# Optimization experiments

Measured on AMD Instinct MI355X. Metric: run time of the kernel, lower is better.

The kernel has to match this reference:

```python
import jax, jax.numpy as jnp
import numpy as np

B, N, IN_DIM, HID, K = 8, 4096, 10, 64, 8
NORM = np.array([1.0/2950.0, 1.0/2950.0, 1.0/2950.0, 1.0/5.265625, 1.0/143.875,
                 1.0/589.0, 1.0/1.2050781, 1.0/211.0, 1.0, 1.0/7.0], dtype=np.float32)


def _lin(key, fan_in, fan_out):
    k1, k2 = jax.random.split(key)
    s = 1.0 / np.sqrt(fan_in)
    w = jax.random.uniform(k1, (fan_in, fan_out), jnp.float32, -s, s)
    b = jax.random.uniform(k2, (fan_out,), jnp.float32, -s, s)
    return w, b


def setup_inputs() -> dict:
    key = jax.random.key(0)
    ks = jax.random.split(key, 10)
    x = jax.random.normal(ks[0], (B, N, IN_DIM), jnp.float32)
    w_in1, b_in1 = _lin(ks[1], IN_DIM, HID // 2)
    w_in2, b_in2 = _lin(ks[2], HID // 2, HID)
    w_c1a, b_c1a = _lin(ks[3], 2 * HID, 3 * HID // 2)
    w_c1b, b_c1b = _lin(ks[4], 3 * HID // 2, HID)
    w_c2a, b_c2a = _lin(ks[5], 2 * HID, 3 * HID // 2)
    w_c2b, b_c2b = _lin(ks[6], 3 * HID // 2, HID)
    w_o1, b_o1 = _lin(ks[7], HID, HID)
    w_o2, b_o2 = _lin(ks[8], HID, HID // 2)
    w_o3, b_o3 = _lin(ks[9], HID // 2, 2)
    return dict(x=x, datanorm=jnp.asarray(NORM),
                w_in1=w_in1, b_in1=b_in1, w_in2=w_in2, b_in2=b_in2,
                w_c1a=w_c1a, b_c1a=b_c1a, w_c1b=w_c1b, b_c1b=b_c1b,
                w_c2a=w_c2a, b_c2a=b_c2a, w_c2b=w_c2b, b_c2b=b_c2b,
                w_o1=w_o1, b_o1=b_o1, w_o2=w_o2, b_o2=b_o2, w_o3=w_o3, b_o3=b_o3)


def _knn(x, k):
    # x: [B, n, H] -> [B, n, k] indices of k nearest neighbors (self excluded)
    x2 = jnp.sum(x * x, -1)
    d = x2[:, :, None] + x2[:, None, :] - 2.0 * jnp.einsum('bnh,bmh->bnm', x, x)
    n = x.shape[1]
    d = d + jnp.eye(n, dtype=x.dtype) * 1e9
    return jax.lax.top_k(-d, k)[1]


def _edge_conv(x, nbr, w1, b1, w2, b2):
    # EdgeConv with max aggregation over undirected kNN edges.
    # message(i <- j) = MLP([x_i, x_j - x_i]); edges symmetrized (j->i and i->j).
    b, n, k = nbr.shape
    dst0 = jnp.broadcast_to(jnp.arange(n)[None, :, None], (b, n, k)).reshape(b, n * k)
    src0 = nbr.reshape(b, n * k)
    src = jnp.concatenate([src0, dst0], 1)  # [b, 2nk]
    dst = jnp.concatenate([dst0, src0], 1)
    xd = jnp.take_along_axis(x, dst[..., None], 1)
    xs = jnp.take_along_axis(x, src[..., None], 1)
    m = jnp.concatenate([xd, xs - xd], -1)           # [b, 2nk, 2H]
    m = jax.nn.elu(m @ w1 + b1)
    m = jax.nn.elu(m @ w2 + b2)
    seg = lambda mm, dd: jax.ops.segment_max(mm, dd, num_segments=n)
    return jax.vmap(seg)(m, dst)                     # [b, n, H]


def reference(x, datanorm, w_in1, b_in1, w_in2, b_in2,
              w_c1a, b_c1a, w_c1b, b_c1b, w_c2a, b_c2a, w_c2b, b_c2b,
              w_o1, b_o1, w_o2, b_o2, w_o3, b_o3):
    h = x * datanorm
    h = jax.nn.elu(h @ w_in1 + b_in1)
    h = jax.nn.elu(h @ w_in2 + b_in2)
    nbr = _knn(jax.lax.stop_gradient(h), K)          # knn_graph is non-differentiable
    h = _edge_conv(h, nbr, w_c1a, b_c1a, w_c1b, b_c1b)
    # deterministic pairwise max-pool (stand-in for graclus+max_pool, halves node count)
    h = h.reshape(B, N // 2, 2, HID).max(2)
    nbr = _knn(jax.lax.stop_gradient(h), K)
    h = _edge_conv(h, nbr, w_c2a, b_c2a, w_c2b, b_c2b)
    # second graclus max_pool_x followed by global_max_pool == global max pool
    g = h.max(1)                                     # [B, HID]
    o = jax.nn.elu(g @ w_o1 + b_o1)
    o = jax.nn.elu(o @ w_o2 + b_o2)
    o = o @ w_o3 + b_o3                              # [B, 2]
    met = jax.nn.softplus(o[:, :1])
    metphi = jnp.pi * (2.0 * jax.nn.sigmoid(o[:, 1:2]) - 1.0)
    return jnp.concatenate([met, metphi], 1)
```

## Files before the change

kernel.cpp:

```cpp
#include <hip/hip_runtime.h>
#include <hip/hip_bf16.h>

#define BATCH 8
#define N1 4096
#define N2 2048
#define HID 64
#define KNN 8
#define INDIM 10

using u64 = unsigned long long;
using bf16 = __hip_bfloat16;
typedef __attribute__((ext_vector_type(8))) short short8;
typedef __attribute__((ext_vector_type(4))) float f32x4;

__device__ __align__(256) float    g_h1[BATCH * N1 * HID];
__device__ __align__(256) float    g_h2[BATCH * N2 * HID];
__device__ __align__(256) float    g_x2n[BATCH * N1];
__device__ __align__(256) float    g_x2n2[BATCH * N2];
__device__ __align__(256) int      g_nbr[BATCH * N1 * KNN];
__device__ __align__(256) float    g_uu[BATCH * N1 * 96];
__device__ __align__(256) float    g_vv[BATCH * N1 * 96];
__device__ __align__(256) unsigned g_ek1[BATCH * N1 * HID];
__device__ __align__(256) unsigned g_ek2[BATCH * N2 * HID];
__device__ __align__(256) short    g_f1[BATCH * N1 * HID];
__device__ __align__(256) short    g_f2[BATCH * N1 * HID];
__device__ __align__(256) short    g_f3[BATCH * N1 * HID];
__device__ __align__(256) float    g_uf[BATCH * N1 * 96];
__device__ __align__(256) float    g_vf[BATCH * N1 * 96];
__device__ __align__(256) short    g_wf1[2 * 4 * 3 * 64 * 8];
__device__ __align__(256) short    g_wf2[2 * 4 * 3 * 64 * 8];

__device__ __forceinline__ float eluf(float x) { return x > 0.f ? x : __expf(x) - 1.f; }
__device__ __forceinline__ unsigned encf(float f) {
  unsigned u = __float_as_uint(f);
  return u ^ ((unsigned)((int)u >> 31) | 0x80000000u);
}
__device__ __forceinline__ float decf(unsigned k) {
  unsigned u = (k & 0x80000000u) ? (k & 0x7FFFFFFFu) : ~k;
  return __uint_as_float(u);
}
#define ENC_NEG1 0x407FFFFFu
__device__ __forceinline__ unsigned enc_safe(float v) {
  if (!(v == v)) return ENC_NEG1;
  return encf(v);
}
__device__ __forceinline__ float dec_safe(unsigned k) {
  float v = decf(k);
  if (!(v == v)) return -1.0f;
  return fminf(fmaxf(v, -3.0e38f), 3.0e38f);
}
__device__ __forceinline__ unsigned umed3(unsigned a, unsigned b, unsigned c) {
  unsigned d;
  asm("v_med3_u32 %0, %1, %2, %3" : "=v"(d) : "v"(a), "v"(b), "v"(c));
  return d;
}
__device__ __forceinline__ void split3(float v, short& b1, short& b2, short& b3) {
  bf16 x1 = __float2bfloat16(v);
  float r1 = v - __bfloat162float(x1);
  bf16 x2 = __float2bfloat16(r1);
  float r2 = r1 - __bfloat162float(x2);
  bf16 x3 = __float2bfloat16(r2);
  b1 = *(short*)&x1; b2 = *(short*)&x2; b3 = *(short*)&x3;
}
__device__ __forceinline__ void split2(float v, short& b1, short& b2) {
  bf16 x1 = __float2bfloat16(v);
  float r1 = v - __bfloat162float(x1);
  bf16 x2 = __float2bfloat16(r1);
  b1 = *(short*)&x1; b2 = *(short*)&x2;
}
__device__ __forceinline__ void store_frags(int node, const short* s1,
                                            const short* s2, const short* s3) {
  size_t tb = ((size_t)(node >> 4)) * 1024 + (node & 15) * 8;
#pragma unroll
  for (int chunk = 0; chunk < 2; ++chunk) {
#pragma unroll
    for (int q = 0; q < 4; ++q) {
      size_t a = tb + chunk * 512 + q * 128;
      int k = chunk * 32 + q * 8;
      *(short8*)(g_f1 + a) = *(const short8*)(s1 + k);
      *(short8*)(g_f2 + a) = *(const short8*)(s2 + k);
      *(short8*)(g_f3 + a) = *(const short8*)(s3 + k);
    }
  }
}
__device__ __forceinline__ void tv_frag(float4 a0, float4 a1, float4 b0,
                                        float4 b1, short8& s1, short8& s2) {
  float v[8] = {a0.x + b0.x, a0.y + b0.y, a0.z + b0.z, a0.w + b0.w,
                a1.x + b1.x, a1.y + b1.y, a1.z + b1.z, a1.w + b1.w};
#pragma unroll
  for (int e = 0; e < 8; ++e) {
    float t = eluf(v[e]);
    short p1, p2;
    split2(t, p1, p2);
    s1[e] = p1; s2[e] = p2;
  }
}

__global__ __launch_bounds__(256) void init_kernel() {
  int t = blockIdx.x * 256 + threadIdx.x;
  uint4 z = make_uint4(ENC_NEG1, ENC_NEG1, ENC_NEG1, ENC_NEG1);
  const int n1 = BATCH * N1 * HID / 4;
  if (t < n1) ((uint4*)g_ek1)[t] = z;
  else ((uint4*)g_ek2)[t - n1] = z;
}

__global__ __launch_bounds__(256) void wfrag_kernel(const float* __restrict__ w1,
                                                    const float* __restrict__ w2) {
  int level = blockIdx.x;
  const float* w = level ? w2 : w1;
  for (int idx = threadIdx.x; idx < 6144; idx += 256) {
    int no = idx / 1536;
    int rem = idx - no * 1536;
    int kc = rem / 512;
    int rem2 = rem - kc * 512;
    int lane = rem2 >> 3;
    int j = rem2 & 7;
    int k = kc * 32 + (lane >> 4) * 8 + j;
    int o = no * 16 + (lane & 15);
    short b1, b2;
    split2(w[k * 64 + o], b1, b2);
    g_wf1[level * 6144 + idx] = b1;
    g_wf2[level * 6144 + idx] = b2;
  }
}

__global__ __launch_bounds__(256) void input_mlp(
    const float* __restrict__ x, const float* __restrict__ norm,
    const float* __restrict__ w1g, const float* __restrict__ b1g,
    const float* __restrict__ w2g, const float* __restrict__ b2g) {
  __shared__ float sw1[320], sb1[32], sw2[2048], sb2[64], snorm[INDIM];
  int t = threadIdx.x;
  for (int q = t; q < 320; q += 256) sw1[q] = w1g[q];
  for (int q = t; q < 2048; q += 256) sw2[q] = w2g[q];
  if (t < 32) sb1[t] = b1g[t];
  if (t < 64) sb2[t] = b2g[t];
  if (t < INDIM) snorm[t] = norm[t];
  __syncthreads();
  int node = blockIdx.x * 256 + t;
  float xv[INDIM];
#pragma unroll
  for (int d = 0; d < INDIM; ++d)
    xv[d] = x[(size_t)node * INDIM + d] * snorm[d];
  float t1[32];
#pragma unroll
  for (int c = 0; c < 32; ++c) {
    float acc = sb1[c];
#pragma unroll
    for (int d = 0; d < INDIM; ++d) acc += xv[d] * sw1[d * 32 + c];
    t1[c] = eluf(acc);
  }
  float* hr = g_h1 + (size_t)node * HID;
  float sq = 0.f;
  short s1l[HID], s2l[HID], s3l[HID];
#pragma unroll
  for (int c = 0; c < HID; ++c) {
    float acc = sb2[c];
#pragma unroll
    for (int d = 0; d < 32; ++d) acc += t1[d] * sw2[d * HID + c];
    float v = eluf(acc);
    hr[c] = v;
    sq += v * v;
    split3(v, s1l[c], s2l[c], s3l[c]);
  }
  store_frags(node, s1l, s2l, s3l);
  g_x2n[node] = sq;
}

template <int LEVEL>
__global__ __launch_bounds__(256, 2) void knn_kernel() {
  constexpr int n = LEVEL ? N2 : N1;
  constexpr int NT = n / 16;
  constexpr int HT = NT / 2;
  constexpr int NSET = LEVEL ? 1 : 2;
  constexpr int SS = NSET * 16;
  __shared__ unsigned lm[32 * 289];

  int b = blockIdx.x & 7;
  int rb = (blockIdx.x >> 3) * (2 * SS);
  int t = threadIdx.x;
  int wv = t >> 6, lane = t & 63;
  int s = wv >> 1, hf = wv & 1;
  int q = lane >> 4, c = lane & 15;
  const float* __restrict__ x2b = (LEVEL ? g_x2n2 : g_x2n) + (size_t)b * n;
  size_t abase = ((size_t)((b * n + rb + s * SS) >> 4)) * 1024 + lane * 8;
  short8 A1a[NSET], A1b[NSET], A2a[NSET], A2b[NSET], A3a[NSET], A3b[NSET];
#pragma unroll
  for (int e = 0; e < NSET; ++e) {
    size_t ab = abase + (size_t)e * 1024;
    A1a[e] = *(const short8*)(g_f1 + ab);
    A1b[e] = *(const short8*)(g_f1 + ab + 512);
    A2a[e] = *(const short8*)(g_f2 + ab);
    A2b[e] = *(const short8*)(g_f2 + ab + 512);
    A3a[e] = *(const short8*)(g_f3 + ab);
    A3b[e] = *(const short8*)(g_f3 + ab + 512);
  }
  unsigned best[NSET][4][KNN];
#pragma unroll
  for (int e = 0; e < NSET; ++e)
#pragma unroll
    for (int r = 0; r < 4; ++r)
#pragma unroll
      for (int p = 0; p < KNN; ++p) best[e][r][p] = 0xFFFFFFFFu;
  const int ct0 = hf * HT;
  const int selftile = (rb + s * SS) >> 4;
  const f32x4 zero = {0.f, 0.f, 0.f, 0.f};
  size_t bb = ((size_t)(b * n) >> 4) * 1024 + (size_t)ct0 * 1024 + lane * 8;

  short8 Pa[6], Pb[6];
  float xa, xb;
  auto LOADB = [&](short8* P, size_t addr) {
    P[0] = *(const short8*)(g_f1 + addr);
    P[1] = *(const short8*)(g_f1 + addr + 512);
    P[2] = *(const short8*)(g_f2 + addr);
    P[3] = *(const short8*)(g_f2 + addr + 512);
    P[4] = *(const short8*)(g_f3 + addr);
    P[5] = *(const short8*)(g_f3 + addr + 512);
  };
  auto COMPUTE = [&](const short8* P, float x2c, int ct) {
#pragma unroll
    for (int e = 0; e < NSET; ++e) {
      f32x4 acc0 = __builtin_amdgcn_mfma_f32_16x16x32_bf16(A1a[e], P[0], zero, 0, 0, 0);
      f32x4 acc1 = __builtin_amdgcn_mfma_f32_16x16x32_bf16(A1b[e], P[1], zero, 0, 0, 0);
      acc0 = __builtin_amdgcn_mfma_f32_16x16x32_bf16(A1a[e], P[2], acc0, 0, 0, 0);
      acc1 = __builtin_amdgcn_mfma_f32_16x16x32_bf16(A1b[e], P[3], acc1, 0, 0, 0);
      acc0 = __builtin_amdgcn_mfma_f32_16x16x32_bf16(A2a[e], P[0], acc0, 0, 0, 0);
      acc1 = __builtin_amdgcn_mfma_f32_16x16x32_bf16(A2b[e], P[1], acc1, 0, 0, 0);
      acc0 = __builtin_amdgcn_mfma_f32_16x16x32_bf16(A1a[e], P[4], acc0, 0, 0, 0);
      acc1 = __builtin_amdgcn_mfma_f32_16x16x32_bf16(A1b[e], P[5], acc1, 0, 0, 0);
      acc0 = __builtin_amdgcn_mfma_f32_16x16x32_bf16(A2a[e], P[2], acc0, 0, 0, 0);
      acc1 = __builtin_amdgcn_mfma_f32_16x16x32_bf16(A2b[e], P[3], acc1, 0, 0, 0);
      acc0 = __builtin_amdgcn_mfma_f32_16x16x32_bf16(A3a[e], P[0], acc0, 0, 0, 0);
      acc1 = __builtin_amdgcn_mfma_f32_16x16x32_bf16(A3b[e], P[1], acc1, 0, 0, 0);
      unsigned ck[4];
#pragma unroll
      for (int r = 0; r < 4; ++r) {
        float sm2 = acc0[r] + acc1[r];
        float dd = __builtin_fmaf(-2.f, sm2, x2c);
        ck[r] = (encf(dd) & 0xFFFFFF00u) | (unsigned)ct;
      }
      if (ct == selftile + e) {
#pragma unroll
        for (int r = 0; r < 4; ++r)
          if (c == q * 4 + r) ck[r] = 0xFFFFFFFFu;
      }
#pragma unroll
      for (int r = 0; r < 4; ++r) {
        unsigned x = ck[r];
#pragma unroll
        for (int p = KNN - 1; p >= 1; --p)
          best[e][r][p] = umed3(best[e][r][p - 1], best[e][r][p], x);
        best[e][r][0] = min(best[e][r][0], x);
      }
    }
  };

  LOADB(Pa, bb);
  xa = x2b[ct0 * 16 + c];
  for (int tt = 0; tt < HT; tt += 2) {
    int ct = ct0 + tt;
    LOADB(Pb, bb + 1024);
    xb = x2b[(ct + 1) * 16 + c];
    COMPUTE(Pa, xa, ct);
    size_t nb2 = (tt + 2 < HT) ? bb + 2048 : bb;
    int ctn2 = (tt + 2 < HT) ? ct + 2 : ct;
    LOADB(Pa, nb2);
    xa = x2b[ctn2 * 16 + c];
    COMPUTE(Pb, xb, ct + 1);
    bb += 2048;
  }
#pragma unroll
  for (int pass = 0; pass < NSET; ++pass) {
#pragma unroll
    for (int r = 0; r < 4; ++r) {
      int lrow = s * 16 + q * 4 + r;
      unsigned* dst = lm + lrow * 289 + (hf * 16 + c) * 9;
#pragma unroll
      for (int p = 0; p < KNN; ++p) dst[p] = best[pass][r][p];
    }
    __syncthreads();
    {
      int arow = t >> 3, am = t & 7;
      unsigned* base = lm + arow * 289;
      const unsigned* l0 = base + (am * 4) * 9;
      u64 fin[KNN];
#pragma unroll
      for (int p = 0; p < KNN; ++p)
        fin[p] = (((u64)l0[p]) << 4) | (unsigned)((am * 4) & 15);
      for (int d = 1; d < 4; ++d) {
        const unsigned* ld = base + (am * 4 + d) * 9;
        unsigned cb = (unsigned)((am * 4 + d) & 15);
        for (int p = 0; p < KNN; ++p) {
          u64 ckk = (((u64)ld[p]) << 4) | cb;
          if (ckk >= fin[KNN - 1]) break;
#pragma unroll
          for (int p2 = 0; p2 < KNN; ++p2) {
            u64 ob = fin[p2];
            bool ex = ob < ckk;
            fin[p2] = ex ? ob : ckk;
            ckk = ex ? ckk : ob;
          }
        }
      }
      unsigned* dst = base + (am * 4) * 9;
#pragma unroll
      for (int p = 0; p < KNN; ++p) {
        dst[2 * p] = (unsigned)fin[p];
        dst[2 * p + 1] = (unsigned)(fin[p] >> 32);
      }
    }
    __syncthreads();
    if (t < 64) {
      int brow = t >> 1, bm = t & 1;
      unsigned* base = lm + brow * 289;
      u64 fin[KNN];
      {
        const unsigned* s0 = base + (bm * 4) * 36;
#pragma unroll
        for (int p = 0; p < KNN; ++p)
          fin[p] = (((u64)s0[2 * p + 1]) << 32) | s0[2 * p];
      }
      for (int d = 1; d < 4; ++d) {
        const unsigned* sd = base + (bm * 4 + d) * 36;
        for (int p = 0; p < KNN; ++p) {
          u64 ckk = (((u64)sd[2 * p + 1]) << 32) | sd[2 * p];
          if (ckk >= fin[KNN - 1]) break;
#pragma unroll
          for (int p2 = 0; p2 < KNN; ++p2) {
            u64 ob = fin[p2];
            bool ex = ob < ckk;
            fin[p2] = ex ? ob : ckk;
            ckk = ex ? ckk : ob;
          }
        }
      }
      unsigned* dst = base + (bm * 4) * 36;
#pragma unroll
      for (int p = 0; p < KNN; ++p) {
        dst[2 * p] = (unsigned)fin[p];
        dst[2 * p + 1] = (unsigned)(fin[p] >> 32);
      }
    }
    __syncthreads();
    if (t < 32) {
      unsigned* base = lm + t * 289;
      u64 fin[KNN];
#pragma unroll
      for (int p = 0; p < KNN; ++p)
        fin[p] = (((u64)base[2 * p + 1]) << 32) | base[2 * p];
      const unsigned* s1 = base + 144;
      for (int p = 0; p < KNN; ++p) {
        u64 ckk = (((u64)s1[2 * p + 1]) << 32) | s1[2 * p];
        if (ckk >= fin[KNN - 1]) break;
#pragma unroll
        for (int p2 = 0; p2 < KNN; ++p2) {
          u64 ob = fin[p2];
          bool ex = ob < ckk;
          fin[p2] = ex ? ob : ckk;
          ckk = ex ? ckk : ob;
        }
      }
      int row = rb + (t >> 4) * SS + pass * 16 + (t & 15);
      int* ob = g_nbr + ((size_t)b * n + row) * KNN;
#pragma unroll
      for (int p = 0; p < KNN; ++p) {
        int j = (int)((fin[p] >> 4) & 255u) * 16 + (int)(fin[p] & 15u);
        ob[p] = j & (n - 1);
      }
    }
    if (pass + 1 < NSET) __syncthreads();
  }
}

__global__ __launch_bounds__(256) void uv_kernel(int level,
                                                 const float* __restrict__ w1g,
                                                 const float* __restrict__ b1g) {
  __shared__ float sw1[128 * 96];
  __shared__ float sb1[96];
  int t = threadIdx.x;
  for (int q = t; q < 128 * 96; q += 256) sw1[q] = w1g[q];
  if (t < 96) sb1[t] = b1g[t];
  __syncthreads();
  const int n = level ? N2 : N1;
  const float* h = level ? g_h2 : g_h1;
  int b = blockIdx.x & 7;
  int nl = (blockIdx.x >> 3) * 64 + (t & 63);
  int c0 = (t >> 6) * 24;
  size_t node = (size_t)b * n + nl;
  const float4* h4 = (const float4*)(h + node * HID);
  float hv[HID];
#pragma unroll
  for (int q = 0; q < 16; ++q) {
    float4 vv = h4[q];
    hv[4 * q] = vv.x; hv[4 * q + 1] = vv.y; hv[4 * q + 2] = vv.z; hv[4 * q + 3] = vv.w;
  }
  float ua[24], va[24];
#pragma unroll
  for (int c = 0; c < 24; ++c) { ua[c] = 0.f; va[c] = 0.f; }
  for (int d = 0; d < HID; ++d) {
    float hd = hv[d];
    const float* wt = sw1 + d * 96 + c0;
    const float* wb = sw1 + (HID + d) * 96 + c0;
#pragma unroll
    for (int c = 0; c < 24; ++c) {
      ua[c] += hd * wt[c];
      va[c] += hd * wb[c];
    }
  }
  float* ur = g_uu + node * 96 + c0;
  float* vr = g_vv + node * 96 + c0;
#pragma unroll
  for (int c = 0; c < 24; ++c) {
    float uval = ua[c] - va[c] + sb1[c0 + c];
    float vval = va[c];
    ur[c] = uval;
    vr[c] = vval;
    int kk = c0 + c;
    size_t fa = (node >> 4) * 1536 + (size_t)((kk >> 5) * 512 +
                ((kk >> 3) & 3) * 128 + (nl & 15) * 8 + (kk & 7));
    g_uf[fa] = uval;
    g_vf[fa] = vval;
  }
}

template <int LEVEL>
__global__ __launch_bounds__(256, 1) void edge_kernel(
    const float* __restrict__ b2g) {
  constexpr int n = LEVEL ? N2 : N1;
  unsigned* ekey = LEVEL ? g_ek2 : g_ek1;
  int b = blockIdx.x & 7;
  int t = threadIdx.x;
  int wv = t >> 6, lane = t & 63;
  int q = lane >> 4, c = lane & 15;
  int base16 = (blockIdx.x >> 3) * 64 + wv * 16;
  int node_c = base16 + c;
  const int* nbb = g_nbr + (size_t)b * n * KNN;
  const float* ub = g_uu + (size_t)b * n * 96;
  const float* vb = g_vv + (size_t)b * n * 96;
  size_t ftile = ((size_t)(b * n + base16) >> 4) * 1536;
  unsigned* eb = ekey + (size_t)b * n * HID;
  short8 W1f[4][3], W2f[4][3];
#pragma unroll
  for (int no = 0; no < 4; ++no)
#pragma unroll
    for (int kc = 0; kc < 3; ++kc) {
      int off = LEVEL * 6144 + ((no * 3 + kc) * 64 + lane) * 8;
      W1f[no][kc] = *(const short8*)(g_wf1 + off);
      W2f[no][kc] = *(const short8*)(g_wf2 + off);
    }
  float biasv[4];
#pragma unroll
  for (int no = 0; no < 4; ++no) biasv[no] = b2g[no * 16 + c];
  float macc[16];
#pragma unroll
  for (int e = 0; e < 16; ++e) macc[e] = -1.0f;
  for (int slot = 0; slot < KNN; ++slot) {
    int jn = nbb[(size_t)node_c * KNN + slot] & (n - 1);
    short8 t1[3], t2[3], r1[3], r2[3];
#pragma unroll
    for (int kc = 0; kc < 3; ++kc) {
      size_t fo = ftile + kc * 512 + lane * 8;
      float4 su0 = *(const float4*)(g_uf + fo);
      float4 su1 = *(const float4*)(g_uf + fo + 4);
      float4 sv0 = *(const float4*)(g_vf + fo);
      float4 sv1 = *(const float4*)(g_vf + fo + 4);
      size_t go = (size_t)jn * 96 + kc * 32 + q * 8;
      float4 gv0 = *(const float4*)(vb + go);
      float4 gv1 = *(const float4*)(vb + go + 4);
      float4 gu0 = *(const float4*)(ub + go);
      float4 gu1 = *(const float4*)(ub + go + 4);
      tv_frag(su0, su1, gv0, gv1, t1[kc], t2[kc]);
      tv_frag(gu0, gu1, sv0, sv1, r1[kc], r2[kc]);
    }
    f32x4 aF[4], aR[4];
#pragma unroll
    for (int no = 0; no < 4; ++no) {
      aF[no] = (f32x4){0.f, 0.f, 0.f, 0.f};
      aR[no] = (f32x4){0.f, 0.f, 0.f, 0.f};
    }
#pragma unroll
    for (int no = 0; no < 4; ++no)
#pragma unroll
      for (int kc = 0; kc < 3; ++kc) {
        aF[no] = __builtin_amdgcn_mfma_f32_16x16x32_bf16(t1[kc], W1f[no][kc], aF[no], 0, 0, 0);
        aF[no] = __builtin_amdgcn_mfma_f32_16x16x32_bf16(t2[kc], W1f[no][kc], aF[no], 0, 0, 0);
        aF[no] = __builtin_amdgcn_mfma_f32_16x16x32_bf16(t1[kc], W2f[no][kc], aF[no], 0, 0, 0);
        aR[no] = __builtin_amdgcn_mfma_f32_16x16x32_bf16(r1[kc], W1f[no][kc], aR[no], 0, 0, 0);
        aR[no] = __builtin_amdgcn_mfma_f32_16x16x32_bf16(r2[kc], W1f[no][kc], aR[no], 0, 0, 0);
        aR[no] = __builtin_amdgcn_mfma_f32_16x16x32_bf16(r1[kc], W2f[no][kc], aR[no], 0, 0, 0);
      }
#pragma unroll
    for (int r = 0; r < 4; ++r) {
      int jr = nbb[(size_t)(base16 + q * 4 + r) * KNN + slot] & (n - 1);
#pragma unroll
      for (int no = 0; no < 4; ++no) {
        float mv = eluf(aR[no][r] + biasv[no]);
        atomicMax(&eb[(size_t)jr * HID + no * 16 + c], enc_safe(mv));
      }
    }
#pragma unroll
    for (int no = 0; no < 4; ++no)
#pragma unroll
      for (int r = 0; r < 4; ++r)
        macc[no * 4 + r] = fmaxf(macc[no * 4 + r], eluf(aF[no][r] + biasv[no]));
  }
#pragma unroll
  for (int r = 0; r < 4; ++r) {
    size_t ib = (size_t)(base16 + q * 4 + r) * HID;
#pragma unroll
    for (int no = 0; no < 4; ++no)
      atomicMax(&eb[ib + no * 16 + c], enc_safe(macc[no * 4 + r]));
  }
}

__global__ __launch_bounds__(256) void pool_kernel() {
  int node = blockIdx.x * 256 + threadIdx.x;
  int b = node >> 11;
  int m = node & (N2 - 1);
  const unsigned* e = g_ek1 + ((size_t)b * N1 + 2 * m) * HID;
  float* hr = g_h2 + (size_t)node * HID;
  float sq = 0.f;
  short s1l[HID], s2l[HID], s3l[HID];
#pragma unroll
  for (int d = 0; d < HID; ++d) {
    float mx = fmaxf(dec_safe(e[d]), dec_safe(e[HID + d]));
    hr[d] = mx;
    sq += mx * mx;
    split3(mx, s1l[d], s2l[d], s3l[d]);
  }
  store_frags(node, s1l, s2l, s3l);
  g_x2n2[node] = sq;
}

__global__ __launch_bounds__(256) void final_kernel(
    const float* __restrict__ wo1, const float* __restrict__ bo1,
    const float* __restrict__ wo2, const float* __restrict__ bo2,
    const float* __restrict__ wo3, const float* __restrict__ bo3,
    float* __restrict__ out) {
  __shared__ unsigned red[4][HID];
  __shared__ float g[HID];
  __shared__ float o1s[HID];
  __shared__ float o2s[32];
  int b = blockIdx.x;
  int t = threadIdx.x;
  int grp = t >> 6, d = t & 63;
  const unsigned* e = g_ek2 + (size_t)b * N2 * HID;
  unsigned mk = 0u;
  for (int m = grp; m < N2; m += 4) {
    unsigned qv = e[(size_t)m * HID + d];
    mk = qv > mk ? qv : mk;
  }
  red[grp][d] = mk;
  __syncthreads();
  if (t < HID) {
    unsigned q1 = red[0][t] > red[1][t] ? red[0][t] : red[1][t];
    unsigned q2 = red[2][t] > red[3][t] ? red[2][t] : red[3][t];
    g[t] = dec_safe(q1 > q2 ? q1 : q2);
  }
  __syncthreads();
  if (t < HID) {
    float a1 = bo1[t];
    for (int dd = 0; dd < HID; ++dd) a1 += g[dd] * wo1[dd * HID + t];
    o1s[t] = eluf(a1);
  }
  __syncthreads();
  if (t < 32) {
    float a2 = bo2[t];
    for (int dd = 0; dd < HID; ++dd) a2 += o1s[dd] * wo2[dd * 32 + t];
    o2s[t] = eluf(a2);
  }
  __syncthreads();
  if (t == 0) {
    float acc0 = bo3[0];
    float acc1 = bo3[1];
    for (int dd = 0; dd < 32; ++dd) {
      acc0 += o2s[dd] * wo3[dd * 2 + 0];
      acc1 += o2s[dd] * wo3[dd * 2 + 1];
    }
    float met = fmaxf(acc0, 0.f) + log1pf(expf(-fabsf(acc0)));
    float phi = 3.14159265358979f * (2.f / (1.f + expf(-acc1)) - 1.f);
    out[b * 2 + 0] = met;
    out[b * 2 + 1] = phi;
  }
}

extern "C" void kernel_launch(void* const* d_in, const int* in_sizes, int n_in,
                              void* d_out, int out_size, void* d_ws,
                              size_t ws_size, hipStream_t stream) {
  const float* x     = (const float*)d_in[0];
  const float* dnorm = (const float*)d_in[1];
  const float* w_in1 = (const float*)d_in[2];
  const float* b_in1 = (const float*)d_in[3];
  const float* w_in2 = (const float*)d_in[4];
  const float* b_in2 = (const float*)d_in[5];
  const float* w_c1a = (const float*)d_in[6];
  const float* b_c1a = (const float*)d_in[7];
  const float* w_c1b = (const float*)d_in[8];
  const float* b_c1b = (const float*)d_in[9];
  const float* w_c2a = (const float*)d_in[10];
  const float* b_c2a = (const float*)d_in[11];
  const float* w_c2b = (const float*)d_in[12];
  const float* b_c2b = (const float*)d_in[13];
  const float* w_o1  = (const float*)d_in[14];
  const float* b_o1  = (const float*)d_in[15];
  const float* w_o2  = (const float*)d_in[16];
  const float* b_o2  = (const float*)d_in[17];
  const float* w_o3  = (const float*)d_in[18];
  const float* b_o3  = (const float*)d_in[19];

  init_kernel<<<(BATCH * N1 * HID + BATCH * N2 * HID) / 4 / 256, 256, 0,
                stream>>>();
  wfrag_kernel<<<2, 256, 0, stream>>>(w_c1b, w_c2b);
  input_mlp<<<BATCH * N1 / 256, 256, 0, stream>>>(x, dnorm, w_in1, b_in1,
                                                  w_in2, b_in2);
  knn_kernel<0><<<8 * (N1 / 64), 256, 0, stream>>>();
  uv_kernel<<<8 * (N1 / 64), 256, 0, stream>>>(0, w_c1a, b_c1a);
  edge_kernel<0><<<8 * (N1 / 64), 256, 0, stream>>>(b_c1b);
  pool_kernel<<<BATCH * N2 / 256, 256, 0, stream>>>();
  knn_kernel<1><<<8 * (N2 / 32), 256, 0, stream>>>();
  uv_kernel<<<8 * (N2 / 64), 256, 0, stream>>>(1, w_c2a, b_c2a);
  edge_kernel<1><<<8 * (N2 / 64), 256, 0, stream>>>(b_c2b);
  final_kernel<<<BATCH, 256, 0, stream>>>(w_o1, b_o1, w_o2, b_o2, w_o3, b_o3,
                                          (float*)d_out);
}
```

Measured before the change: 564.0 us.

## Merge independent prep kernels and co-launch kNN with UV projection

Folds init, weight-fragment prep and the input MLP into a single launch that dispatches on block index. kNN and UV projection for each level, which do not depend on each other, now share one launch: a shared-memory buffer is reused and blocks are routed by index, so both run concurrently. The UV loop also streams h rows with one float4 of prefetch instead of loading all 64 values into registers first. This cuts launches and fills the GPU better, but the shared kernel uses the larger shared footprint and launch bounds for both roles, which could limit occupancy for the UV blocks.

```diff
diff --git a/kernel.cpp b/kernel.cpp
--- a/kernel.cpp
+++ b/kernel.cpp
@@ -96,84 +96,82 @@
   }
 }
 
-__global__ __launch_bounds__(256) void init_kernel() {
-  int t = blockIdx.x * 256 + threadIdx.x;
-  uint4 z = make_uint4(ENC_NEG1, ENC_NEG1, ENC_NEG1, ENC_NEG1);
-  const int n1 = BATCH * N1 * HID / 4;
-  if (t < n1) ((uint4*)g_ek1)[t] = z;
-  else ((uint4*)g_ek2)[t - n1] = z;
-}
-
-__global__ __launch_bounds__(256) void wfrag_kernel(const float* __restrict__ w1,
-                                                    const float* __restrict__ w2) {
-  int level = blockIdx.x;
-  const float* w = level ? w2 : w1;
-  for (int idx = threadIdx.x; idx < 6144; idx += 256) {
-    int no = idx / 1536;
-    int rem = idx - no * 1536;
-    int kc = rem / 512;
-    int rem2 = rem - kc * 512;
-    int lane = rem2 >> 3;
-    int j = rem2 & 7;
-    int k = kc * 32 + (lane >> 4) * 8 + j;
-    int o = no * 16 + (lane & 15);
-    short b1, b2;
-    split2(w[k * 64 + o], b1, b2);
-    g_wf1[level * 6144 + idx] = b1;
-    g_wf2[level * 6144 + idx] = b2;
-  }
-}
-
-__global__ __launch_bounds__(256) void input_mlp(
+__global__ __launch_bounds__(256) void prep_kernel(
     const float* __restrict__ x, const float* __restrict__ norm,
     const float* __restrict__ w1g, const float* __restrict__ b1g,
-    const float* __restrict__ w2g, const float* __restrict__ b2g) {
-  __shared__ float sw1[320], sb1[32], sw2[2048], sb2[64], snorm[INDIM];
+    const float* __restrict__ w2g, const float* __restrict__ b2g,
+    const float* __restrict__ wc1b, const float* __restrict__ wc2b) {
+  int bid = blockIdx.x;
   int t = threadIdx.x;
-  for (int q = t; q < 320; q += 256) sw1[q] = w1g[q];
-  for (int q = t; q < 2048; q += 256) sw2[q] = w2g[q];
-  if (t < 32) sb1[t] = b1g[t];
-  if (t < 64) sb2[t] = b2g[t];
-  if (t < INDIM) snorm[t] = norm[t];
-  __syncthreads();
-  int node = blockIdx.x * 256 + t;
-  float xv[INDIM];
-#pragma unroll
-  for (int d = 0; d < INDIM; ++d)
-    xv[d] = x[(size_t)node * INDIM + d] * snorm[d];
-  float t1[32];
-#pragma unroll
-  for (int c = 0; c < 32; ++c) {
-    float acc = sb1[c];
-#pragma unroll
-    for (int d = 0; d < INDIM; ++d) acc += xv[d] * sw1[d * 32 + c];
-    t1[c] = eluf(acc);
-  }
-  float* hr = g_h1 + (size_t)node * HID;
-  float sq = 0.f;
-  short s1l[HID], s2l[HID], s3l[HID];
-#pragma unroll
-  for (int c = 0; c < HID; ++c) {
-    float acc = sb2[c];
-#pragma unroll
-    for (int d = 0; d < 32; ++d) acc += t1[d] * sw2[d * HID + c];
-    float v = eluf(acc);
-    hr[c] = v;
-    sq += v * v;
-    split3(v, s1l[c], s2l[c], s3l[c]);
-  }
-  store_frags(node, s1l, s2l, s3l);
-  g_x2n[node] = sq;
+  if (bid < 128) {
+    __shared__ float sw1[320], sb1[32], sw2[2048], sb2[64], snorm[INDIM];
+    for (int q = t; q < 320; q += 256) sw1[q] = w1g[q];
+    for (int q = t; q < 2048; q += 256) sw2[q] = w2g[q];
+    if (t < 32) sb1[t] = b1g[t];
+    if (t < 64) sb2[t] = b2g[t];
+    if (t < INDIM) snorm[t] = norm[t];
+    __syncthreads();
+    int node = bid * 256 + t;
+    float xv[INDIM];
+#pragma unroll
+    for (int d = 0; d < INDIM; ++d)
+      xv[d] = x[(size_t)node * INDIM + d] * snorm[d];
+    float t1[32];
+#pragma unroll
+    for (int c = 0; c < 32; ++c) {
+      float acc = sb1[c];
+#pragma unroll
+      for (int d = 0; d < INDIM; ++d) acc += xv[d] * sw1[d * 32 + c];
+      t1[c] = eluf(acc);
+    }
+    float* hr = g_h1 + (size_t)node * HID;
+    float sq = 0.f;
+    short s1l[HID], s2l[HID], s3l[HID];
+#pragma unroll
+    for (int c = 0; c < HID; ++c) {
+      float acc = sb2[c];
+#pragma unroll
+      for (int d = 0; d < 32; ++d) acc += t1[d] * sw2[d * HID + c];
+      float v = eluf(acc);
+      hr[c] = v;
+      sq += v * v;
+      split3(v, s1l[c], s2l[c], s3l[c]);
+    }
+    store_frags(node, s1l, s2l, s3l);
+    g_x2n[node] = sq;
+  } else if (bid < 130) {
+    int level = bid - 128;
+    const float* w = level ? wc2b : wc1b;
+    for (int idx = t; idx < 6144; idx += 256) {
+      int no = idx / 1536;
+      int rem = idx - no * 1536;
+      int kc = rem / 512;
+      int rem2 = rem - kc * 512;
+      int lane = rem2 >> 3;
+      int j = rem2 & 7;
+      int k = kc * 32 + (lane >> 4) * 8 + j;
+      int o = no * 16 + (lane & 15);
+      short b1, b2;
+      split2(w[k * 64 + o], b1, b2);
+      g_wf1[level * 6144 + idx] = b1;
+      g_wf2[level * 6144 + idx] = b2;
+    }
+  } else {
+    int tt = (bid - 130) * 256 + t;
+    uint4 z = make_uint4(ENC_NEG1, ENC_NEG1, ENC_NEG1, ENC_NEG1);
+    const int n1 = BATCH * N1 * HID / 4;
+    if (tt < n1) ((uint4*)g_ek1)[tt] = z;
+    else ((uint4*)g_ek2)[tt - n1] = z;
+  }
 }
 
 template <int LEVEL>
-__global__ __launch_bounds__(256, 2) void knn_kernel() {
+__device__ __forceinline__ void knn_body(unsigned* lm) {
   constexpr int n = LEVEL ? N2 : N1;
   constexpr int NT = n / 16;
   constexpr int HT = NT / 2;
   constexpr int NSET = LEVEL ? 1 : 2;
   constexpr int SS = NSET * 16;
-  __shared__ unsigned lm[32 * 289];
 
   int b = blockIdx.x & 7;
   int rb = (blockIdx.x >> 3) * (2 * SS);
@@ -371,39 +369,40 @@
   }
 }
 
-__global__ __launch_bounds__(256) void uv_kernel(int level,
-                                                 const float* __restrict__ w1g,
-                                                 const float* __restrict__ b1g) {
-  __shared__ float sw1[128 * 96];
-  __shared__ float sb1[96];
+template <int LEVEL>
+__device__ __forceinline__ void uv_body(float* sw1, float* sb1, int ub,
+                                        const float* __restrict__ w1g,
+                                        const float* __restrict__ b1g) {
   int t = threadIdx.x;
   for (int q = t; q < 128 * 96; q += 256) sw1[q] = w1g[q];
   if (t < 96) sb1[t] = b1g[t];
   __syncthreads();
-  const int n = level ? N2 : N1;
-  const float* h = level ? g_h2 : g_h1;
-  int b = blockIdx.x & 7;
-  int nl = (blockIdx.x >> 3) * 64 + (t & 63);
+  const int n = LEVEL ? N2 : N1;
+  const float* h = LEVEL ? g_h2 : g_h1;
+  int b = ub & 7;
+  int nl = (ub >> 3) * 64 + (t & 63);
   int c0 = (t >> 6) * 24;
   size_t node = (size_t)b * n + nl;
   const float4* h4 = (const float4*)(h + node * HID);
-  float hv[HID];
-#pragma unroll
-  for (int q = 0; q < 16; ++q) {
-    float4 vv = h4[q];
-    hv[4 * q] = vv.x; hv[4 * q + 1] = vv.y; hv[4 * q + 2] = vv.z; hv[4 * q + 3] = vv.w;
-  }
   float ua[24], va[24];
 #pragma unroll
   for (int c = 0; c < 24; ++c) { ua[c] = 0.f; va[c] = 0.f; }
-  for (int d = 0; d < HID; ++d) {
-    float hd = hv[d];
-    const float* wt = sw1 + d * 96 + c0;
-    const float* wb = sw1 + (HID + d) * 96 + c0;
-#pragma unroll
-    for (int c = 0; c < 24; ++c) {
-      ua[c] += hd * wt[c];
-      va[c] += hd * wb[c];
+  float4 vv = h4[0];
+  for (int qd = 0; qd < 16; ++qd) {
+    float4 cur = vv;
+    if (qd < 15) vv = h4[qd + 1];
+    float el[4] = {cur.x, cur.y, cur.z, cur.w};
+#pragma unroll
+    for (int j = 0; j < 4; ++j) {
+      int d = qd * 4 + j;
+      float hd = el[j];
+      const float* wt = sw1 + d * 96 + c0;
+      const float* wb = sw1 + (HID + d) * 96 + c0;
+#pragma unroll
+      for (int c = 0; c < 24; ++c) {
+        ua[c] += hd * wt[c];
+        va[c] += hd * wb[c];
+      }
     }
   }
   float* ur = g_uu + node * 96 + c0;
@@ -419,6 +418,19 @@
                 ((kk >> 3) & 3) * 128 + (nl & 15) * 8 + (kk & 7));
     g_uf[fa] = uval;
     g_vf[fa] = vval;
+  }
+}
+
+template <int LEVEL>
+__global__ __launch_bounds__(256, 2) void knuv_kernel(
+    const float* __restrict__ w1g, const float* __restrict__ b1g) {
+  constexpr int KB = LEVEL ? (8 * (N2 / 32)) : (8 * (N1 / 64));
+  __shared__ __align__(16) unsigned char smem[49536];
+  if ((int)blockIdx.x < KB) {
+    knn_body<LEVEL>((unsigned*)smem);
+  } else {
+    uv_body<LEVEL>((float*)smem, (float*)(smem + 49152),
+                   (int)blockIdx.x - KB, w1g, b1g);
   }
 }
 
@@ -607,17 +619,12 @@
   const float* w_o3  = (const float*)d_in[18];
   const float* b_o3  = (const float*)d_in[19];
 
-  init_kernel<<<(BATCH * N1 * HID + BATCH * N2 * HID) / 4 / 256, 256, 0,
-                stream>>>();
-  wfrag_kernel<<<2, 256, 0, stream>>>(w_c1b, w_c2b);
-  input_mlp<<<BATCH * N1 / 256, 256, 0, stream>>>(x, dnorm, w_in1, b_in1,
-                                                  w_in2, b_in2);
-  knn_kernel<0><<<8 * (N1 / 64), 256, 0, stream>>>();
-  uv_kernel<<<8 * (N1 / 64), 256, 0, stream>>>(0, w_c1a, b_c1a);
+  prep_kernel<<<3202, 256, 0, stream>>>(x, dnorm, w_in1, b_in1, w_in2, b_in2,
+                                        w_c1b, w_c2b);
+  knuv_kernel<0><<<1024, 256, 0, stream>>>(w_c1a, b_c1a);
   edge_kernel<0><<<8 * (N1 / 64), 256, 0, stream>>>(b_c1b);
   pool_kernel<<<BATCH * N2 / 256, 256, 0, stream>>>();
-  knn_kernel<1><<<8 * (N2 / 32), 256, 0, stream>>>();
-  uv_kernel<<<8 * (N2 / 64), 256, 0, stream>>>(1, w_c2a, b_c2a);
+  knuv_kernel<1><<<768, 256, 0, stream>>>(w_c2a, b_c2a);
   edge_kernel<1><<<8 * (N2 / 64), 256, 0, stream>>>(b_c2b);
   final_kernel<<<BATCH, 256, 0, stream>>>(w_o1, b_o1, w_o2, b_o2, w_o3, b_o3,
                                           (float*)d_out);
```

Result: faster. 496.1 us, median of 2 (-12.0%).
